# Kernel tuning notes

Measured on AMD Instinct MI355X. Metric: run time of the kernel, lower is better.

## Reference

```python
import jax, jax.numpy as jnp
import numpy as np

D_MODEL = 1024
N_HEADS = 16
FF_DIM = 4096
EPS = 1e-05


def setup_inputs() -> dict:
    key = jax.random.key(0)
    ks = jax.random.split(key, 8)
    B, T, E, F = 4, 2048, D_MODEL, FF_DIM
    s = 0.02
    return {
        "encoder_input": jax.random.normal(ks[0], (B, T, E), jnp.float32),
        "source_padding_masks": jax.random.randint(ks[1], (B, T), 0, 2, jnp.int32),
        "Wq": jax.random.normal(ks[2], (E, E), jnp.float32) * s,
        "Wk": jax.random.normal(ks[3], (E, E), jnp.float32) * s,
        "Wv": jax.random.normal(ks[4], (E, E), jnp.float32) * s,
        "Wo": jax.random.normal(ks[5], (E, E), jnp.float32) * s,
        "w1": jax.random.normal(ks[6], (F, E), jnp.float32) * s,
        "b1": jnp.zeros((F,), jnp.float32),
        "w2": jax.random.normal(ks[7], (E, F), jnp.float32) * s,
        "b2": jnp.zeros((E,), jnp.float32),
        "ln_g": jnp.ones((E,), jnp.float32),
        "ln_b": jnp.zeros((E,), jnp.float32),
    }


def _layer_norm(x, g, b):
    # Faithful to the custom LayerNorm: unbiased std (ddof=1), eps added to sd.
    mean = jnp.mean(x, axis=-1, keepdims=True)
    sd = jnp.std(x, axis=-1, keepdims=True, ddof=1)
    return (x - mean) / (sd + EPS) * g + b


def reference(encoder_input, source_padding_masks, Wq, Wk, Wv, Wo, w1, b1, w2, b2, ln_g, ln_b):
    x = encoder_input
    B, T, E = x.shape
    H, hd = N_HEADS, E // N_HEADS

    q = (x @ Wq.T).reshape(B, T, H, hd).transpose(0, 2, 1, 3)  # [B,H,T,hd]
    k = (x @ Wk.T).reshape(B, T, H, hd).transpose(0, 2, 1, 3)
    v = (x @ Wv.T).reshape(B, T, H, hd).transpose(0, 2, 1, 3)

    scores = jnp.einsum("bhqd,bhkd->bhqk", q, k) / jnp.sqrt(jnp.float32(hd))
    key_mask = source_padding_masks[:, None, None, :]  # [B,1,1,T]
    scores = jnp.where(key_mask == 0, -jnp.inf, scores)
    attn = jax.nn.softmax(scores, axis=-1)
    attn = attn * source_padding_masks[:, None, :, None].astype(attn.dtype)  # query mask post-softmax

    ctx = jnp.einsum("bhqk,bhkd->bhqd", attn, v)
    ctx = ctx.transpose(0, 2, 1, 3).reshape(B, T, E)
    att_out = ctx @ Wo.T

    # residual block 1 (dropout is identity in eval)
    h = _layer_norm(att_out + x, ln_g, ln_b)

    ff = jax.nn.relu(h @ w1.T + b1) @ w2.T + b2
    # residual block 2 (same shared LayerNorm params)
    out = _layer_norm(ff + h, ln_g, ln_b)
    return out
```

## Files before the change

kernel.cpp:

```cpp
#include <hip/hip_runtime.h>
#include <hip/hip_bf16.h>


typedef __attribute__((ext_vector_type(8))) short  short8;
typedef __attribute__((ext_vector_type(4))) float  f32x4;
typedef __attribute__((ext_vector_type(4))) int    i32x4;
typedef __attribute__((ext_vector_type(4))) unsigned short u16x4;

__device__ inline float b2f(unsigned short u) {
    unsigned int x = ((unsigned int)u) << 16;
    return __builtin_bit_cast(float, x);
}
__device__ inline unsigned short f2b(float f) {
    return __builtin_bit_cast(unsigned short, __float2bfloat16(f));
}

__device__ inline void llds16(const unsigned short* g, unsigned short* l) {
    __builtin_amdgcn_global_load_lds(
        (const __attribute__((address_space(1))) unsigned int*)g,
        (__attribute__((address_space(3))) unsigned int*)l, 16, 0, 0);
}

__device__ inline int swz(int row, int col8) {
    return (row << 6) + (((col8 ^ (row >> 1)) & 7) << 3);
}

struct CastArgs {
    const float* src[7];
    unsigned short* dst[7];
    int blkcum[8];
};

__global__ __launch_bounds__(256)
void cast_all(CastArgs a)
{
    int blk = blockIdx.x;
    int s = 0;
    while (blk >= a.blkcum[s + 1]) ++s;
    int i = (blk - a.blkcum[s]) * 256 + threadIdx.x;
    f32x4 v = *(const f32x4*)(a.src[s] + (size_t)i * 4);
    u16x4 o;
    for (int j = 0; j < 4; ++j) o[j] = f2b(v[j]);
    *(u16x4*)(a.dst[s] + (size_t)i * 4) = o;
}

__global__ __launch_bounds__(256)
void mask_bf16(const int* __restrict__ m, unsigned short* __restrict__ mb, int n)
{
    int i = blockIdx.x * 256 + threadIdx.x;
    if (i < n) mb[i] = m[i] ? (unsigned short)0x3F80 : (unsigned short)0;
}

template <int BIAS, int RELU, int QKV>
__global__ __launch_bounds__(256, 2)
void gemm_db(const unsigned short* __restrict__ A,
             const unsigned short* __restrict__ W,
             const float* __restrict__ bias,
             const int* __restrict__ mask,
             unsigned short* __restrict__ C0,
             unsigned short* __restrict__ C1,
             unsigned short* __restrict__ C2,
             int M, int N, int K)
{
    __shared__ __attribute__((aligned(16))) unsigned short a_s[2][128 * 64];
    __shared__ __attribute__((aligned(16))) unsigned short b_s[2][128 * 64];

    const int tid  = threadIdx.x;
    const int lane = tid & 63;
    const int w    = tid >> 6;
    const int ln   = lane & 15;
    const int quad = lane >> 4;
    const int wm   = w >> 1, wn = w & 1;
    const int bm   = blockIdx.y, bn = blockIdx.x;

    f32x4 acc[4][4] = {};

    const unsigned short* Abase = A + (size_t)(bm * 128) * K;
    const unsigned short* Wbase = W + (size_t)(bn * 128) * K;

    auto stage = [&](int buf, int kt) {
#pragma unroll
        for (int i = 0; i < 4; ++i) {
            int e   = i * 256 + tid;
            int row = e >> 3;
            int c8  = (e & 7) ^ ((e >> 4) & 7);
            llds16(Abase + (size_t)row * K + kt * 64 + c8 * 8, &a_s[buf][e * 8]);
            llds16(Wbase + (size_t)row * K + kt * 64 + c8 * 8, &b_s[buf][e * 8]);
        }
    };

    const int nkt = K >> 6;
    stage(0, 0);
    stage(1, 1);
    int cur = 0;
    for (int kt = 0; kt < nkt; ++kt) {
        if (kt + 1 < nkt) asm volatile("s_waitcnt vmcnt(8)" ::: "memory");
        else              asm volatile("s_waitcnt vmcnt(0)" ::: "memory");
        asm volatile("s_barrier" ::: "memory");
#pragma unroll
        for (int ks = 0; ks < 2; ++ks) {
            short8 af[4], bf_[4];
#pragma unroll
            for (int mt = 0; mt < 4; ++mt)
                af[mt] = *(const short8*)&a_s[cur][swz(wm * 64 + mt * 16 + ln, ks * 4 + quad)];
#pragma unroll
            for (int nt = 0; nt < 4; ++nt)
                bf_[nt] = *(const short8*)&b_s[cur][swz(wn * 64 + nt * 16 + ln, ks * 4 + quad)];
#pragma unroll
            for (int mt = 0; mt < 4; ++mt)
#pragma unroll
                for (int nt = 0; nt < 4; ++nt)
                    acc[mt][nt] = __builtin_amdgcn_mfma_f32_16x16x32_bf16(
                        af[mt], bf_[nt], acc[mt][nt], 0, 0, 0);
        }
        asm volatile("s_barrier" ::: "memory");
        if (kt + 2 < nkt) stage(cur, kt + 2);
        cur ^= 1;
    }

    if (QKV) {
        const int seg = bn >> 3;
        const int lbn = bn & 7;
        if (seg < 2) {
            unsigned short* C = seg == 0 ? C0 : C1;
            const float scl = seg == 0 ? 0.18033688f : 1.0f;
#pragma unroll
            for (int nt = 0; nt < 4; ++nt) {
                int col = lbn * 128 + wn * 64 + nt * 16 + ln;
#pragma unroll
                for (int mt = 0; mt < 4; ++mt) {
                    int row0 = bm * 128 + wm * 64 + mt * 16 + quad * 4;
#pragma unroll
                    for (int r = 0; r < 4; ++r)
                        C[(size_t)(row0 + r) * 1024 + col] = f2b(acc[mt][nt][r] * scl);
                }
            }
        } else {
            const int T2 = 2048, H2 = 16;
#pragma unroll
            for (int mt = 0; mt < 4; ++mt) {
                int row0 = bm * 128 + wm * 64 + mt * 16 + quad * 4;
                int bb = row0 >> 11, t0 = row0 & 2047;
                i32x4 mi = *(const i32x4*)&mask[bb * 2048 + t0];
#pragma unroll
                for (int nt = 0; nt < 4; ++nt) {
                    int col = lbn * 128 + wn * 64 + nt * 16 + ln;
                    int hh2 = col >> 6, d = col & 63;
                    u16x4 o;
#pragma unroll
                    for (int r = 0; r < 4; ++r)
                        o[r] = mi[r] ? f2b(acc[mt][nt][r]) : (unsigned short)0;
                    *(u16x4*)(C2 + ((size_t)((bb * H2 + hh2) * 64 + d)) * T2 + t0) = o;
                }
            }
        }
    } else {
#pragma unroll
        for (int nt = 0; nt < 4; ++nt) {
            int col = bn * 128 + wn * 64 + nt * 16 + ln;
            float bv = 0.f;
            if (BIAS) bv = bias[col];
#pragma unroll
            for (int mt = 0; mt < 4; ++mt) {
                int row0 = bm * 128 + wm * 64 + mt * 16 + quad * 4;
#pragma unroll
                for (int r = 0; r < 4; ++r) {
                    float v = acc[mt][nt][r] + bv;
                    if (RELU) v = v > 0.f ? v : 0.f;
                    C0[(size_t)(row0 + r) * N + col] = f2b(v);
                }
            }
        }
    }
}

__global__ __launch_bounds__(512, 2)
void flash_attn6(const unsigned short* __restrict__ Q,
                 const unsigned short* __restrict__ K,
                 const unsigned short* __restrict__ Vt,
                 const unsigned short* __restrict__ mb,
                 const int* __restrict__ mask,
                 unsigned short* __restrict__ O,
                 int T, int H, int E)
{
    __shared__ __attribute__((aligned(16))) unsigned short k_s[2][64 * 64];
    __shared__ __attribute__((aligned(16))) unsigned short v_s[2][64 * 64];
    __shared__ __attribute__((aligned(16))) unsigned short p_s[8][512];

    const int ord = blockIdx.x;
    const int wg  = (ord & 7) * 128 + (ord >> 3);
    const int qt  = wg & 15;
    const int h   = (wg >> 4) & 15;
    const int b   = wg >> 8;

    const int tid  = threadIdx.x;
    const int w    = tid >> 6;
    const int lane = tid & 63;
    const int ln   = lane & 15;
    const int quad = lane >> 4;
    const int q0   = qt * 128;
    const unsigned short* vt_b = Vt + (size_t)(b * H + h) * 64 * T;

    const unsigned short* qp = Q + (size_t)(b * T + q0 + w * 16 + ln) * E + h * 64;
    short8 aq[2];
    aq[0] = *(const short8*)(qp + quad * 8);
    aq[1] = *(const short8*)(qp + 32 + quad * 8);

    {
        int e = tid;
        int row = e >> 3;
        int c8  = (e & 7) ^ ((e >> 4) & 7);
        llds16(K + (size_t)(b * T + row) * E + h * 64 + c8 * 8, &k_s[0][e * 8]);
        llds16(vt_b + (size_t)row * T + c8 * 8, &v_s[0][e * 8]);
    }
    __syncthreads();

    f32x4 Oa[4] = {};
    f32x4 lacc = {};
    unsigned short* ph = &p_s[w][0];
    const int rdoff = ln * 32 + (((quad ^ (ln >> 1)) & 3) << 3);

    const int nkb = T >> 6;
    for (int kb = 0; kb < nkb; ++kb) {
        const int cur = kb & 1;
        if (kb + 1 < nkb) {
            int e = tid;
            int row = e >> 3;
            int c8  = (e & 7) ^ ((e >> 4) & 7);
            llds16(K + (size_t)(b * T + (kb + 1) * 64 + row) * E + h * 64 + c8 * 8,
                   &k_s[cur ^ 1][e * 8]);
            llds16(vt_b + (size_t)row * T + (kb + 1) * 64 + c8 * 8,
                   &v_s[cur ^ 1][e * 8]);
        }
        short8 mf0 = *(const short8*)&mb[b * T + kb * 64 + quad * 8];
        short8 mf1 = *(const short8*)&mb[b * T + kb * 64 + 32 + quad * 8];

        f32x4 S[4] = {};
        for (int ks = 0; ks < 2; ++ks)
            for (int nt = 0; nt < 4; ++nt) {
                short8 bf_ = *(const short8*)&k_s[cur][swz(nt * 16 + ln, ks * 4 + quad)];
                S[nt] = __builtin_amdgcn_mfma_f32_16x16x32_bf16(aq[ks], bf_, S[nt], 0, 0, 0);
            }

        for (int nt = 0; nt < 2; ++nt)
            for (int r = 0; r < 4; ++r) {
                float p = exp2f(S[nt][r]);
                int qr = quad * 4 + r;
                int k8 = 2 * nt + (ln >> 3);
                ph[qr * 32 + (((k8 ^ (qr >> 1)) & 3) << 3) + (ln & 7)] = f2b(p);
            }
        short8 ap0 = *(const short8*)&ph[rdoff];
        lacc = __builtin_amdgcn_mfma_f32_16x16x32_bf16(ap0, mf0, lacc, 0, 0, 0);
        for (int nt = 0; nt < 4; ++nt) {
            short8 bv0 = *(const short8*)&v_s[cur][swz(nt * 16 + ln, quad)];
            Oa[nt] = __builtin_amdgcn_mfma_f32_16x16x32_bf16(ap0, bv0, Oa[nt], 0, 0, 0);
        }
        for (int nt = 0; nt < 2; ++nt)
            for (int r = 0; r < 4; ++r) {
                float p = exp2f(S[2 + nt][r]);
                int qr = quad * 4 + r;
                int k8 = 2 * nt + (ln >> 3);
                ph[qr * 32 + (((k8 ^ (qr >> 1)) & 3) << 3) + (ln & 7)] = f2b(p);
            }
        short8 ap1 = *(const short8*)&ph[rdoff];
        lacc = __builtin_amdgcn_mfma_f32_16x16x32_bf16(ap1, mf1, lacc, 0, 0, 0);
        for (int nt = 0; nt < 4; ++nt) {
            short8 bv1 = *(const short8*)&v_s[cur][swz(nt * 16 + ln, 4 + quad)];
            Oa[nt] = __builtin_amdgcn_mfma_f32_16x16x32_bf16(ap1, bv1, Oa[nt], 0, 0, 0);
        }
        __syncthreads();
    }

    for (int r = 0; r < 4; ++r) {
        int qrow = q0 + w * 16 + quad * 4 + r;
        float inv = mask[b * T + qrow] ? 1.f / lacc[r] : 0.f;
        for (int nt = 0; nt < 4; ++nt)
            O[(size_t)(b * T + qrow) * E + h * 64 + nt * 16 + ln] = f2b(Oa[nt][r] * inv);
    }
}

template <int R_F32, int O_F32>
__global__ __launch_bounds__(256, 4)
void ln_residual(const unsigned short* __restrict__ A,
                 const void* __restrict__ R,
                 const float* __restrict__ G,
                 const float* __restrict__ Bt,
                 void* __restrict__ Y, int E)
{
    const int row = blockIdx.x;
    const int tid = threadIdx.x;
    size_t base = (size_t)row * E + tid * 4;
    u16x4 a4 = *(const u16x4*)(A + base);
    float rv[4];
    if (R_F32) {
        f32x4 r4 = *(const f32x4*)((const float*)R + base);
        for (int j = 0; j < 4; ++j) rv[j] = r4[j];
    } else {
        u16x4 r4 = *(const u16x4*)((const unsigned short*)R + base);
        for (int j = 0; j < 4; ++j) rv[j] = b2f(r4[j]);
    }
    float v[4]; float s = 0.f, sq = 0.f;
    for (int j = 0; j < 4; ++j) {
        v[j] = b2f(a4[j]) + rv[j];
        s += v[j]; sq += v[j] * v[j];
    }
    for (int o = 32; o; o >>= 1) {
        s  += __shfl_xor(s, o, 64);
        sq += __shfl_xor(sq, o, 64);
    }
    __shared__ float red[8];
    int w = tid >> 6, lane = tid & 63;
    if (lane == 0) { red[w] = s; red[4 + w] = sq; }
    __syncthreads();
    s  = red[0] + red[1] + red[2] + red[3];
    sq = red[4] + red[5] + red[6] + red[7];
    float mean = s / E;
    float var  = (sq - s * mean) / (E - 1);
    var = fmaxf(var, 0.f);
    float inv = 1.f / (sqrtf(var) + 1e-5f);
    f32x4 g4 = *(const f32x4*)(G + tid * 4);
    f32x4 b4 = *(const f32x4*)(Bt + tid * 4);
    if (O_F32) {
        f32x4 o4;
        for (int j = 0; j < 4; ++j)
            o4[j] = (v[j] - mean) * inv * g4[j] + b4[j];
        *(f32x4*)((float*)Y + base) = o4;
    } else {
        u16x4 o4;
        for (int j = 0; j < 4; ++j)
            o4[j] = f2b((v[j] - mean) * inv * g4[j] + b4[j]);
        *(u16x4*)((unsigned short*)Y + base) = o4;
    }
}

extern "C" void kernel_launch(void* const* d_in, const int* in_sizes, int n_in,
                              void* d_out, int out_size, void* d_ws, size_t ws_size,
                              hipStream_t stream)
{
    const int B = 4, T = 2048, E = 1024, F = 4096, H = 16;
    const int M = B * T;

    const float* x  = (const float*)d_in[0];
    const int* mask = (const int*)d_in[1];
    const float* Wq = (const float*)d_in[2];
    const float* Wk = (const float*)d_in[3];
    const float* Wv = (const float*)d_in[4];
    const float* Wo = (const float*)d_in[5];
    const float* w1 = (const float*)d_in[6];
    const float* b1 = (const float*)d_in[7];
    const float* w2 = (const float*)d_in[8];
    const float* b2 = (const float*)d_in[9];
    const float* lg = (const float*)d_in[10];
    const float* lb = (const float*)d_in[11];
    float* out = (float*)d_out;

    char* ws = (char*)d_ws;
    const size_t MB = 1024 * 1024;
    unsigned short* xb  = (unsigned short*)(ws);
    unsigned short* q   = (unsigned short*)(ws + 16 * MB);
    unsigned short* kk  = (unsigned short*)(ws + 32 * MB);
    unsigned short* vt  = (unsigned short*)(ws + 48 * MB);
    unsigned short* ctx = (unsigned short*)(ws + 64 * MB);
    unsigned short* hh  = (unsigned short*)(ws + 80 * MB);
    unsigned short* mbf = hh;
    unsigned short* ff1 = (unsigned short*)(ws);
    unsigned short* ff2 = ctx;
    unsigned short* att = q;
    unsigned short* Wqb = (unsigned short*)(ws + 96 * MB);
    unsigned short* Wkb = (unsigned short*)(ws + 98 * MB);
    unsigned short* Wvb = (unsigned short*)(ws + 100 * MB);
    unsigned short* Wob = (unsigned short*)(ws + 102 * MB);
    unsigned short* w1b = (unsigned short*)(ws + 104 * MB);
    unsigned short* w2b = (unsigned short*)(ws + 112 * MB);

    dim3 blk(256);
    dim3 g512(512);

    CastArgs ca;
    ca.src[0] = x;  ca.dst[0] = xb;
    ca.src[1] = Wq; ca.dst[1] = Wqb;
    ca.src[2] = Wk; ca.dst[2] = Wkb;
    ca.src[3] = Wv; ca.dst[3] = Wvb;
    ca.src[4] = Wo; ca.dst[4] = Wob;
    ca.src[5] = w1; ca.dst[5] = w1b;
    ca.src[6] = w2; ca.dst[6] = w2b;
    int blks[7] = { M * E / 1024, E * E / 1024, E * E / 1024, E * E / 1024,
                    E * E / 1024, F * E / 1024, F * E / 1024 };
    ca.blkcum[0] = 0;
    for (int i = 0; i < 7; ++i) ca.blkcum[i + 1] = ca.blkcum[i] + blks[i];
    cast_all<<<dim3(ca.blkcum[7]), blk, 0, stream>>>(ca);
    mask_bf16<<<dim3(M / 256), blk, 0, stream>>>(mask, mbf, M);

    gemm_db<0, 0, 1><<<dim3(3072 / 128, M / 128), blk, 0, stream>>>(
        xb, Wqb, nullptr, mask, q, kk, vt, M, 3072, E);
    flash_attn6<<<dim3((T / 128) * H * B), g512, 0, stream>>>(q, kk, vt, mbf, mask, ctx, T, H, E);
    gemm_db<0, 0, 0><<<dim3(E / 128, M / 128), blk, 0, stream>>>(
        ctx, Wob, nullptr, nullptr, att, nullptr, nullptr, M, E, E);
    ln_residual<1, 0><<<dim3(M), blk, 0, stream>>>(att, x, lg, lb, hh, E);
    gemm_db<1, 1, 0><<<dim3(F / 128, M / 128), blk, 0, stream>>>(
        hh, w1b, b1, nullptr, ff1, nullptr, nullptr, M, F, E);
    gemm_db<1, 0, 0><<<dim3(E / 128, M / 128), blk, 0, stream>>>(
        ff1, w2b, b2, nullptr, ff2, nullptr, nullptr, M, E, F);
    ln_residual<0, 1><<<dim3(M), blk, 0, stream>>>(ff2, hh, lg, lb, out, E);
}
```

Baseline: 505.3 us.

## Fold mask conversion into cast kernel, add MFMA priority hints, faster bf16 rounding

Moves the int-mask-to-bf16 conversion into the existing batched cast kernel, which saves one kernel launch. Wraps the MFMA blocks in the GEMM and attention kernels with s_setprio so matrix work gets issue priority over other waves. Replaces the library float-to-bf16 conversion in attention with a manual round-to-nearest-even bit trick, which cuts instructions but does not handle NaN specially.

```diff
diff --git a/kernel.cpp b/kernel.cpp
--- a/kernel.cpp
+++ b/kernel.cpp
@@ -14,6 +14,11 @@
 __device__ inline unsigned short f2b(float f) {
     return __builtin_bit_cast(unsigned short, __float2bfloat16(f));
 }
+__device__ inline unsigned short f2b_fast(float f) {
+    unsigned int x = __builtin_bit_cast(unsigned int, f);
+    x += 0x7FFF + ((x >> 16) & 1);
+    return (unsigned short)(x >> 16);
+}
 
 __device__ inline void llds16(const unsigned short* g, unsigned short* l) {
     __builtin_amdgcn_global_load_lds(
@@ -26,9 +31,9 @@
 }
 
 struct CastArgs {
-    const float* src[7];
-    unsigned short* dst[7];
-    int blkcum[8];
+    const void* src[8];
+    unsigned short* dst[8];
+    int blkcum[9];
 };
 
 __global__ __launch_bounds__(256)
@@ -38,17 +43,16 @@
     int s = 0;
     while (blk >= a.blkcum[s + 1]) ++s;
     int i = (blk - a.blkcum[s]) * 256 + threadIdx.x;
-    f32x4 v = *(const f32x4*)(a.src[s] + (size_t)i * 4);
     u16x4 o;
-    for (int j = 0; j < 4; ++j) o[j] = f2b(v[j]);
+    if (s == 7) {
+        i32x4 m = *(const i32x4*)((const int*)a.src[s] + (size_t)i * 4);
+        for (int j = 0; j < 4; ++j)
+            o[j] = m[j] ? (unsigned short)0x3F80 : (unsigned short)0;
+    } else {
+        f32x4 v = *(const f32x4*)((const float*)a.src[s] + (size_t)i * 4);
+        for (int j = 0; j < 4; ++j) o[j] = f2b(v[j]);
+    }
     *(u16x4*)(a.dst[s] + (size_t)i * 4) = o;
-}
-
-__global__ __launch_bounds__(256)
-void mask_bf16(const int* __restrict__ m, unsigned short* __restrict__ mb, int n)
-{
-    int i = blockIdx.x * 256 + threadIdx.x;
-    if (i < n) mb[i] = m[i] ? (unsigned short)0x3F80 : (unsigned short)0;
 }
 
 template <int BIAS, int RELU, int QKV>
@@ -106,12 +110,14 @@
 #pragma unroll
             for (int nt = 0; nt < 4; ++nt)
                 bf_[nt] = *(const short8*)&b_s[cur][swz(wn * 64 + nt * 16 + ln, ks * 4 + quad)];
+            __builtin_amdgcn_s_setprio(1);
 #pragma unroll
             for (int mt = 0; mt < 4; ++mt)
 #pragma unroll
                 for (int nt = 0; nt < 4; ++nt)
                     acc[mt][nt] = __builtin_amdgcn_mfma_f32_16x16x32_bf16(
                         af[mt], bf_[nt], acc[mt][nt], 0, 0, 0);
+            __builtin_amdgcn_s_setprio(0);
         }
         asm volatile("s_barrier" ::: "memory");
         if (kt + 2 < nkt) stage(cur, kt + 2);
@@ -236,38 +242,44 @@
         short8 mf1 = *(const short8*)&mb[b * T + kb * 64 + 32 + quad * 8];
 
         f32x4 S[4] = {};
+        __builtin_amdgcn_s_setprio(1);
         for (int ks = 0; ks < 2; ++ks)
             for (int nt = 0; nt < 4; ++nt) {
                 short8 bf_ = *(const short8*)&k_s[cur][swz(nt * 16 + ln, ks * 4 + quad)];
                 S[nt] = __builtin_amdgcn_mfma_f32_16x16x32_bf16(aq[ks], bf_, S[nt], 0, 0, 0);
             }
+        __builtin_amdgcn_s_setprio(0);
 
         for (int nt = 0; nt < 2; ++nt)
             for (int r = 0; r < 4; ++r) {
                 float p = exp2f(S[nt][r]);
                 int qr = quad * 4 + r;
                 int k8 = 2 * nt + (ln >> 3);
-                ph[qr * 32 + (((k8 ^ (qr >> 1)) & 3) << 3) + (ln & 7)] = f2b(p);
+                ph[qr * 32 + (((k8 ^ (qr >> 1)) & 3) << 3) + (ln & 7)] = f2b_fast(p);
             }
         short8 ap0 = *(const short8*)&ph[rdoff];
+        __builtin_amdgcn_s_setprio(1);
         lacc = __builtin_amdgcn_mfma_f32_16x16x32_bf16(ap0, mf0, lacc, 0, 0, 0);
         for (int nt = 0; nt < 4; ++nt) {
             short8 bv0 = *(const short8*)&v_s[cur][swz(nt * 16 + ln, quad)];
             Oa[nt] = __builtin_amdgcn_mfma_f32_16x16x32_bf16(ap0, bv0, Oa[nt], 0, 0, 0);
         }
+        __builtin_amdgcn_s_setprio(0);
         for (int nt = 0; nt < 2; ++nt)
             for (int r = 0; r < 4; ++r) {
                 float p = exp2f(S[2 + nt][r]);
                 int qr = quad * 4 + r;
                 int k8 = 2 * nt + (ln >> 3);
-                ph[qr * 32 + (((k8 ^ (qr >> 1)) & 3) << 3) + (ln & 7)] = f2b(p);
+                ph[qr * 32 + (((k8 ^ (qr >> 1)) & 3) << 3) + (ln & 7)] = f2b_fast(p);
             }
         short8 ap1 = *(const short8*)&ph[rdoff];
+        __builtin_amdgcn_s_setprio(1);
         lacc = __builtin_amdgcn_mfma_f32_16x16x32_bf16(ap1, mf1, lacc, 0, 0, 0);
         for (int nt = 0; nt < 4; ++nt) {
             short8 bv1 = *(const short8*)&v_s[cur][swz(nt * 16 + ln, 4 + quad)];
             Oa[nt] = __builtin_amdgcn_mfma_f32_16x16x32_bf16(ap1, bv1, Oa[nt], 0, 0, 0);
         }
+        __builtin_amdgcn_s_setprio(0);
         __syncthreads();
     }
 
@@ -275,7 +287,7 @@
         int qrow = q0 + w * 16 + quad * 4 + r;
         float inv = mask[b * T + qrow] ? 1.f / lacc[r] : 0.f;
         for (int nt = 0; nt < 4; ++nt)
-            O[(size_t)(b * T + qrow) * E + h * 64 + nt * 16 + ln] = f2b(Oa[nt][r] * inv);
+            O[(size_t)(b * T + qrow) * E + h * 64 + nt * 16 + ln] = f2b_fast(Oa[nt][r] * inv);
     }
 }
 
@@ -377,19 +389,19 @@
     dim3 g512(512);
 
     CastArgs ca;
-    ca.src[0] = x;  ca.dst[0] = xb;
-    ca.src[1] = Wq; ca.dst[1] = Wqb;
-    ca.src[2] = Wk; ca.dst[2] = Wkb;
-    ca.src[3] = Wv; ca.dst[3] = Wvb;
-    ca.src[4] = Wo; ca.dst[4] = Wob;
-    ca.src[5] = w1; ca.dst[5] = w1b;
-    ca.src[6] = w2; ca.dst[6] = w2b;
-    int blks[7] = { M * E / 1024, E * E / 1024, E * E / 1024, E * E / 1024,
-                    E * E / 1024, F * E / 1024, F * E / 1024 };
+    ca.src[0] = x;    ca.dst[0] = xb;
+    ca.src[1] = Wq;   ca.dst[1] = Wqb;
+    ca.src[2] = Wk;   ca.dst[2] = Wkb;
+    ca.src[3] = Wv;   ca.dst[3] = Wvb;
+    ca.src[4] = Wo;   ca.dst[4] = Wob;
+    ca.src[5] = w1;   ca.dst[5] = w1b;
+    ca.src[6] = w2;   ca.dst[6] = w2b;
+    ca.src[7] = mask; ca.dst[7] = mbf;
+    int blks[8] = { M * E / 1024, E * E / 1024, E * E / 1024, E * E / 1024,
+                    E * E / 1024, F * E / 1024, F * E / 1024, M / 1024 };
     ca.blkcum[0] = 0;
-    for (int i = 0; i < 7; ++i) ca.blkcum[i + 1] = ca.blkcum[i] + blks[i];
-    cast_all<<<dim3(ca.blkcum[7]), blk, 0, stream>>>(ca);
-    mask_bf16<<<dim3(M / 256), blk, 0, stream>>>(mask, mbf, M);
+    for (int i = 0; i < 8; ++i) ca.blkcum[i + 1] = ca.blkcum[i] + blks[i];
+    cast_all<<<dim3(ca.blkcum[8]), blk, 0, stream>>>(ca);
 
     gemm_db<0, 0, 1><<<dim3(3072 / 128, M / 128), blk, 0, stream>>>(
         xb, Wqb, nullptr, mask, q, kk, vt, M, 3072, E);
```

Result: slower. 524.8 us (+3.9%).
